# Kernel tuning notes

Measured on AMD Instinct MI355X. Metric: run time of the kernel, lower is better.

The kernel has to match this reference:

```python
import jax, jax.numpy as jnp
import numpy as np

N_NODES = 100000
N_EDGES = 1600000
D_IN = 128
D_OUT = 128


def setup_inputs() -> dict:
    key = jax.random.key(0)
    k = jax.random.split(key, 6)
    x = jax.random.normal(k[0], (N_NODES, D_IN), dtype=jnp.float32)
    edge_src = jax.random.randint(k[1], (N_EDGES,), 0, N_NODES, dtype=jnp.int64)
    edge_dst = jax.random.randint(k[2], (N_EDGES,), 0, N_NODES, dtype=jnp.int64)
    edge_weight = jax.random.uniform(k[3], (N_EDGES,), dtype=jnp.float32)
    # xavier-uniform-ish init for the two projection matrices
    lim = float(np.sqrt(6.0 / (D_IN + D_OUT)))
    W_nbrs = jax.random.uniform(k[4], (D_IN, D_OUT), minval=-lim, maxval=lim, dtype=jnp.float32)
    W_self = jax.random.uniform(k[5], (D_IN, D_OUT), minval=-lim, maxval=lim, dtype=jnp.float32)
    bias = jnp.zeros((D_OUT,), dtype=jnp.float32)
    return {"x": x, "edge_src": edge_src, "edge_dst": edge_dst,
            "edge_weight": edge_weight, "W_nbrs": W_nbrs, "W_self": W_self,
            "bias": bias}


def reference(x, edge_src, edge_dst, edge_weight, W_nbrs, W_self, bias):
    # y = x @ W_nbrs  (dense projection)
    y = x @ W_nbrs                                   # [N, D_OUT]
    # spmm(adj, y): out[i] = sum_{(j->i) in E} w_ij * y[j]
    msgs = edge_weight[:, None] * y[edge_src]        # [E, D_OUT]
    agg = jax.ops.segment_sum(msgs, edge_dst, num_segments=x.shape[0])
    # self transform + bias
    return agg + x @ W_self + bias
```

## Files before the change

### kernel.cpp

```cpp
#include <hip/hip_runtime.h>
#include <hip/hip_bf16.h>

#define D 128

typedef __bf16 bf16x8 __attribute__((ext_vector_type(8)));
typedef float f32x4 __attribute__((ext_vector_type(4)));

__device__ __forceinline__ unsigned short f2bf(float f) {
    unsigned u = __float_as_uint(f);
    u += 0x7FFFu + ((u >> 16) & 1u);
    return (unsigned short)(u >> 16);
}
__device__ __forceinline__ float bf2f(unsigned u16) {
    return __uint_as_float(u16 << 16);
}

__global__ void k_build_wt(const float* __restrict__ Wn, const float* __restrict__ Ws,
                           unsigned short* __restrict__ WTs) {
    int g = blockIdx.x * blockDim.x + threadIdx.x;
    int k = g >> 8;
    int c = g & 255;
    float v = (c < 128) ? Wn[k * 128 + c] : Ws[k * 128 + (c - 128)];
    int chunk = k >> 3;
    WTs[c * 128 + (((chunk ^ (c & 15)) << 3) | (k & 7))] = f2bf(v);
}

__global__ __launch_bounds__(256) void k_gemm_rank(
    const float* __restrict__ x, const unsigned short* __restrict__ WTs,
    const float* __restrict__ bias, int N,
    unsigned short* __restrict__ y, float* __restrict__ out,
    const int* __restrict__ edst, int E,
    int* __restrict__ cnt, int* __restrict__ rank) {
    __shared__ unsigned short sm[128 * 128];
    int b = blockIdx.x;
    int tid = threadIdx.x;
    if (b % 5 != 0) {
        int rb = (b / 5) * 4 + (b % 5) - 1;
        int e = rb * 256 + tid;
        if (e < E) {
            int d = edst[e];
            rank[e] = atomicAdd(&cnt[d], 1);
        }
        return;
    }
    int gb = b / 5;
    int w = tid >> 6, l = tid & 63;
    int row0 = gb * 64 + w * 16;
    if (gb * 64 >= N) return;
    int c15 = l & 15;
    int kgrp = l >> 4;
    const uint4* gs = (const uint4*)WTs;
    uint4* ss = (uint4*)sm;
    {
        #pragma unroll
        for (int r = 0; r < 8; ++r) ss[r * 256 + tid] = gs[r * 256 + tid];
    }
    int arow = row0 + c15;
    bool avalid = (arow < N);
    const float* xr = x + (size_t)arow * D;
    bf16x8 afrag[4];
    #pragma unroll
    for (int ks = 0; ks < 4; ++ks) {
        int k0 = ks * 32 + kgrp * 8;
        float4 a0, a1;
        if (avalid) { a0 = *(const float4*)(xr + k0); a1 = *(const float4*)(xr + k0 + 4); }
        else { a0 = make_float4(0.f, 0.f, 0.f, 0.f); a1 = a0; }
        bf16x8 f;
        f[0] = (__bf16)a0.x; f[1] = (__bf16)a0.y; f[2] = (__bf16)a0.z; f[3] = (__bf16)a0.w;
        f[4] = (__bf16)a1.x; f[5] = (__bf16)a1.y; f[6] = (__bf16)a1.z; f[7] = (__bf16)a1.w;
        afrag[ks] = f;
    }
    __syncthreads();
    int orow = row0 + kgrp * 4;
    #pragma unroll
    for (int nt = 0; nt < 8; ++nt) {
        int c = nt * 16 + c15;
        f32x4 acc = {0.f, 0.f, 0.f, 0.f};
        #pragma unroll
        for (int ks = 0; ks < 4; ++ks) {
            int chunk = ks * 4 + kgrp;
            const bf16x8* bp = (const bf16x8*)(sm + c * 128 + ((chunk ^ c15) << 3));
            acc = __builtin_amdgcn_mfma_f32_16x16x32_bf16(afrag[ks], *bp, acc, 0, 0, 0);
        }
        #pragma unroll
        for (int j = 0; j < 4; ++j) {
            int r = orow + j;
            if (r < N) y[(size_t)r * D + c] = f2bf(acc[j]);
        }
    }
    __syncthreads();
    {
        #pragma unroll
        for (int r = 0; r < 8; ++r) ss[r * 256 + tid] = gs[2048 + r * 256 + tid];
    }
    __syncthreads();
    #pragma unroll
    for (int nt = 0; nt < 8; ++nt) {
        int c = nt * 16 + c15;
        f32x4 acc = {0.f, 0.f, 0.f, 0.f};
        #pragma unroll
        for (int ks = 0; ks < 4; ++ks) {
            int chunk = ks * 4 + kgrp;
            const bf16x8* bp = (const bf16x8*)(sm + c * 128 + ((chunk ^ c15) << 3));
            acc = __builtin_amdgcn_mfma_f32_16x16x32_bf16(afrag[ks], *bp, acc, 0, 0, 0);
        }
        float bsv = bias[c];
        #pragma unroll
        for (int j = 0; j < 4; ++j) {
            int r = orow + j;
            if (r < N) out[(size_t)r * D + c] = acc[j] + bsv;
        }
    }
}

__global__ void k_scanA(const int* __restrict__ cnt, int N,
                        int* __restrict__ ofs, int* __restrict__ bsum) {
    __shared__ int lds[1024];
    int t = threadIdx.x, i = blockIdx.x * 1024 + t;
    int v = (i < N) ? cnt[i] : 0;
    lds[t] = v; __syncthreads();
    for (int d = 1; d < 1024; d <<= 1) {
        int x = (t >= d) ? lds[t - d] : 0; __syncthreads();
        lds[t] += x; __syncthreads();
    }
    if (i < N) ofs[i] = lds[t] - v;
    if (t == 1023) bsum[blockIdx.x] = lds[t];
}

__global__ void k_scanB(int* __restrict__ bsum, int NB) {
    __shared__ int lds[128];
    int t = threadIdx.x;
    int v = (t < NB) ? bsum[t] : 0;
    lds[t] = v; __syncthreads();
    for (int d = 1; d < 128; d <<= 1) {
        int x = (t >= d) ? lds[t - d] : 0; __syncthreads();
        lds[t] += x; __syncthreads();
    }
    if (t < NB) bsum[t] = lds[t] - v;
}

__global__ __launch_bounds__(256) void k_fill(
    const int* __restrict__ src, const int* __restrict__ dst,
    const float* __restrict__ w, const int* __restrict__ rank, int E,
    const int* __restrict__ ofs, const int* __restrict__ bsum,
    uint2* __restrict__ sorted) {
    int e = blockIdx.x * blockDim.x + threadIdx.x;
    if (e < E) {
        int d = dst[e];
        int pos = ofs[d] + bsum[d >> 10] + rank[e];
        sorted[pos] = make_uint2((unsigned)src[e], __float_as_uint(w[e]));
    }
}

__global__ __launch_bounds__(256) void k_agg(
    const unsigned short* __restrict__ y, const uint2* __restrict__ sorted,
    const int* __restrict__ ofs, const int* __restrict__ bsum,
    const int* __restrict__ cnt, int N,
    float* __restrict__ out) {
    int w = threadIdx.x >> 6, l = threadIdx.x & 63;
    int node = blockIdx.x * 4 + w;
    if (node >= N) return;
    int s = ofs[node] + bsum[node >> 10], n = cnt[node];
    int g = l >> 4, li = l & 15;
    const uint2* sp = sorted + s;
    float a0 = 0.f, a1 = 0.f, a2 = 0.f, a3 = 0.f;
    float a4 = 0.f, a5 = 0.f, a6 = 0.f, a7 = 0.f;
    int j = g;
    for (; j + 4 < n; j += 8) {
        uint2 pa = sp[j];
        uint2 pb = sp[j + 4];
        uint4 va = *(const uint4*)(y + (size_t)pa.x * D + li * 8);
        uint4 vb = *(const uint4*)(y + (size_t)pb.x * D + li * 8);
        float wa = __uint_as_float(pa.y), wb = __uint_as_float(pb.y);
        a0 += wa * bf2f(va.x & 0xFFFFu); a1 += wa * bf2f(va.x >> 16);
        a2 += wa * bf2f(va.y & 0xFFFFu); a3 += wa * bf2f(va.y >> 16);
        a4 += wa * bf2f(va.z & 0xFFFFu); a5 += wa * bf2f(va.z >> 16);
        a6 += wa * bf2f(va.w & 0xFFFFu); a7 += wa * bf2f(va.w >> 16);
        a0 += wb * bf2f(vb.x & 0xFFFFu); a1 += wb * bf2f(vb.x >> 16);
        a2 += wb * bf2f(vb.y & 0xFFFFu); a3 += wb * bf2f(vb.y >> 16);
        a4 += wb * bf2f(vb.z & 0xFFFFu); a5 += wb * bf2f(vb.z >> 16);
        a6 += wb * bf2f(vb.w & 0xFFFFu); a7 += wb * bf2f(vb.w >> 16);
    }
    if (j < n) {
        uint2 p = sp[j];
        uint4 v = *(const uint4*)(y + (size_t)p.x * D + li * 8);
        float wt = __uint_as_float(p.y);
        a0 += wt * bf2f(v.x & 0xFFFFu); a1 += wt * bf2f(v.x >> 16);
        a2 += wt * bf2f(v.y & 0xFFFFu); a3 += wt * bf2f(v.y >> 16);
        a4 += wt * bf2f(v.z & 0xFFFFu); a5 += wt * bf2f(v.z >> 16);
        a6 += wt * bf2f(v.w & 0xFFFFu); a7 += wt * bf2f(v.w >> 16);
    }
    a0 += __shfl_xor(a0, 16, 64); a1 += __shfl_xor(a1, 16, 64);
    a2 += __shfl_xor(a2, 16, 64); a3 += __shfl_xor(a3, 16, 64);
    a4 += __shfl_xor(a4, 16, 64); a5 += __shfl_xor(a5, 16, 64);
    a6 += __shfl_xor(a6, 16, 64); a7 += __shfl_xor(a7, 16, 64);
    a0 += __shfl_xor(a0, 32, 64); a1 += __shfl_xor(a1, 32, 64);
    a2 += __shfl_xor(a2, 32, 64); a3 += __shfl_xor(a3, 32, 64);
    a4 += __shfl_xor(a4, 32, 64); a5 += __shfl_xor(a5, 32, 64);
    a6 += __shfl_xor(a6, 32, 64); a7 += __shfl_xor(a7, 32, 64);
    if (l < 16) {
        float4* op = (float4*)(out + (size_t)node * D + li * 8);
        float4 o0 = op[0], o1 = op[1];
        o0.x += a0; o0.y += a1; o0.z += a2; o0.w += a3;
        o1.x += a4; o1.y += a5; o1.z += a6; o1.w += a7;
        op[0] = o0; op[1] = o1;
    }
}

extern "C" void kernel_launch(void* const* d_in, const int* in_sizes, int n_in,
                              void* d_out, int out_size, void* d_ws, size_t ws_size,
                              hipStream_t stream) {
    const float* x    = (const float*)d_in[0];
    const int*   esrc = (const int*)d_in[1];
    const int*   edst = (const int*)d_in[2];
    const float* ew   = (const float*)d_in[3];
    const float* Wn   = (const float*)d_in[4];
    const float* Wsf  = (const float*)d_in[5];
    const float* bias = (const float*)d_in[6];
    float* out = (float*)d_out;
    int N = in_sizes[0] / D;
    int E = in_sizes[1];

    char* ws = (char*)d_ws;
    size_t off = 0;
    unsigned short* WTs = (unsigned short*)(ws + off); off += 256 * 128 * sizeof(unsigned short);
    unsigned short* yb  = (unsigned short*)(ws + off); off += (size_t)N * D * sizeof(unsigned short);
    off = (off + 255) & ~(size_t)255;
    int* cnt  = (int*)(ws + off); off += (size_t)N * 4; off = (off + 255) & ~(size_t)255;
    int* ofs  = (int*)(ws + off); off += (size_t)N * 4; off = (off + 255) & ~(size_t)255;
    int* bsum = (int*)(ws + off); off += 1024;
    int* rank = (int*)(ws + off); off += (size_t)E * 4; off = (off + 255) & ~(size_t)255;
    uint2* sorted = (uint2*)(ws + off); off += (size_t)E * 8;

    hipMemsetAsync(cnt, 0, (size_t)N * 4, stream);

    k_build_wt<<<128, 256, 0, stream>>>(Wn, Wsf, WTs);

    int GB = (N + 63) / 64;
    int RB = (E + 255) / 256;
    int G5 = (GB > (RB + 3) / 4 ? GB : (RB + 3) / 4) * 5;
    k_gemm_rank<<<G5, 256, 0, stream>>>(x, WTs, bias, N, yb, out,
                                        edst, E, cnt, rank);

    int NB = (N + 1023) / 1024;
    k_scanA<<<NB, 1024, 0, stream>>>(cnt, N, ofs, bsum);
    k_scanB<<<1, 128, 0, stream>>>(bsum, NB);
    k_fill<<<(E + 255) / 256, 256, 0, stream>>>(esrc, edst, ew, rank, E, ofs, bsum, sorted);

    k_agg<<<(N + 3) / 4, 256, 0, stream>>>(yb, sorted, ofs, bsum, cnt, N, out);
}
```

Measured before the change: 304.0 us.

## Permute bf16 y columns for vector stores and stage output through LDS

The GEMM now stores the bf16 projection y in a permuted column order, so each lane writes 8 contiguous bf16 values as one vector store. The aggregation kernel's read-modify-write of out is changed to the matching strided column mapping. The self-transform output goes through LDS so it can be written with coalesced float4 stores that include the bias. The cnt memset is folded into the weight-transpose kernel, and the GEMM/rank block interleave changes from 1:4 to 1:1, with each rank block handling 1024 edges. The aim is fewer scattered narrow global stores and one fewer launch, at the cost of extra LDS traffic and syncs in the GEMM blocks.

```diff
diff --git a/kernel.cpp b/kernel.cpp
--- a/kernel.cpp
+++ b/kernel.cpp
@@ -4,6 +4,7 @@
 #define D 128
 
 typedef __bf16 bf16x8 __attribute__((ext_vector_type(8)));
+typedef unsigned short u16x8 __attribute__((ext_vector_type(8)));
 typedef float f32x4 __attribute__((ext_vector_type(4)));
 
 __device__ __forceinline__ unsigned short f2bf(float f) {
@@ -16,13 +17,15 @@
 }
 
 __global__ void k_build_wt(const float* __restrict__ Wn, const float* __restrict__ Ws,
-                           unsigned short* __restrict__ WTs) {
+                           unsigned short* __restrict__ WTs,
+                           int* __restrict__ cnt, int N) {
     int g = blockIdx.x * blockDim.x + threadIdx.x;
     int k = g >> 8;
     int c = g & 255;
     float v = (c < 128) ? Wn[k * 128 + c] : Ws[k * 128 + (c - 128)];
     int chunk = k >> 3;
     WTs[c * 128 + (((chunk ^ (c & 15)) << 3) | (k & 7))] = f2bf(v);
+    for (int i = g; i < N; i += 32768) cnt[i] = 0;
 }
 
 __global__ __launch_bounds__(256) void k_gemm_rank(
@@ -34,19 +37,23 @@
     __shared__ unsigned short sm[128 * 128];
     int b = blockIdx.x;
     int tid = threadIdx.x;
-    if (b % 5 != 0) {
-        int rb = (b / 5) * 4 + (b % 5) - 1;
-        int e = rb * 256 + tid;
-        if (e < E) {
-            int d = edst[e];
-            rank[e] = atomicAdd(&cnt[d], 1);
+    if (b & 1) {
+        int e0 = (b >> 1) * 1024 + tid;
+        #pragma unroll
+        for (int k = 0; k < 4; ++k) {
+            int e = e0 + k * 256;
+            if (e < E) {
+                int d = edst[e];
+                rank[e] = atomicAdd(&cnt[d], 1);
+            }
         }
         return;
     }
-    int gb = b / 5;
+    int gb = b >> 1;
+    int brow = gb * 64;
+    if (brow >= N) return;
     int w = tid >> 6, l = tid & 63;
-    int row0 = gb * 64 + w * 16;
-    if (gb * 64 >= N) return;
+    int row0 = brow + w * 16;
     int c15 = l & 15;
     int kgrp = l >> 4;
     const uint4* gs = (const uint4*)WTs;
@@ -72,20 +79,27 @@
     }
     __syncthreads();
     int orow = row0 + kgrp * 4;
+    f32x4 acc[8];
     #pragma unroll
     for (int nt = 0; nt < 8; ++nt) {
         int c = nt * 16 + c15;
-        f32x4 acc = {0.f, 0.f, 0.f, 0.f};
+        f32x4 a = {0.f, 0.f, 0.f, 0.f};
         #pragma unroll
         for (int ks = 0; ks < 4; ++ks) {
             int chunk = ks * 4 + kgrp;
             const bf16x8* bp = (const bf16x8*)(sm + c * 128 + ((chunk ^ c15) << 3));
-            acc = __builtin_amdgcn_mfma_f32_16x16x32_bf16(afrag[ks], *bp, acc, 0, 0, 0);
-        }
-        #pragma unroll
-        for (int j = 0; j < 4; ++j) {
-            int r = orow + j;
-            if (r < N) y[(size_t)r * D + c] = f2bf(acc[j]);
+            a = __builtin_amdgcn_mfma_f32_16x16x32_bf16(afrag[ks], *bp, a, 0, 0, 0);
+        }
+        acc[nt] = a;
+    }
+    #pragma unroll
+    for (int j = 0; j < 4; ++j) {
+        int r = orow + j;
+        if (r < N) {
+            u16x8 f;
+            #pragma unroll
+            for (int nt = 0; nt < 8; ++nt) f[nt] = f2bf(acc[nt][j]);
+            *(u16x8*)(y + (size_t)r * D + c15 * 8) = f;
         }
     }
     __syncthreads();
@@ -97,18 +111,34 @@
     #pragma unroll
     for (int nt = 0; nt < 8; ++nt) {
         int c = nt * 16 + c15;
-        f32x4 acc = {0.f, 0.f, 0.f, 0.f};
+        f32x4 a = {0.f, 0.f, 0.f, 0.f};
         #pragma unroll
         for (int ks = 0; ks < 4; ++ks) {
             int chunk = ks * 4 + kgrp;
             const bf16x8* bp = (const bf16x8*)(sm + c * 128 + ((chunk ^ c15) << 3));
-            acc = __builtin_amdgcn_mfma_f32_16x16x32_bf16(afrag[ks], *bp, acc, 0, 0, 0);
-        }
-        float bsv = bias[c];
-        #pragma unroll
-        for (int j = 0; j < 4; ++j) {
-            int r = orow + j;
-            if (r < N) out[(size_t)r * D + c] = acc[j] + bsv;
+            a = __builtin_amdgcn_mfma_f32_16x16x32_bf16(afrag[ks], *bp, a, 0, 0, 0);
+        }
+        acc[nt] = a;
+    }
+    __syncthreads();
+    float* smf = (float*)sm;
+    int lr0 = w * 16 + kgrp * 4;
+    #pragma unroll
+    for (int nt = 0; nt < 8; ++nt) {
+        #pragma unroll
+        for (int j = 0; j < 4; ++j)
+            smf[(lr0 + j) * 128 + nt * 16 + c15] = acc[nt][j];
+    }
+    __syncthreads();
+    float4 bv = *(const float4*)&bias[(tid * 4) & 127];
+    #pragma unroll
+    for (int k = 0; k < 8; ++k) {
+        int f = tid * 4 + k * 1024;
+        int gr = brow + (f >> 7);
+        if (gr < N) {
+            float4 c4 = *(float4*)&smf[f];
+            c4.x += bv.x; c4.y += bv.y; c4.z += bv.z; c4.w += bv.w;
+            *(float4*)(out + (size_t)brow * D + f) = c4;
         }
     }
 }
@@ -199,11 +229,9 @@
     a4 += __shfl_xor(a4, 32, 64); a5 += __shfl_xor(a5, 32, 64);
     a6 += __shfl_xor(a6, 32, 64); a7 += __shfl_xor(a7, 32, 64);
     if (l < 16) {
-        float4* op = (float4*)(out + (size_t)node * D + li * 8);
-        float4 o0 = op[0], o1 = op[1];
-        o0.x += a0; o0.y += a1; o0.z += a2; o0.w += a3;
-        o1.x += a4; o1.y += a5; o1.z += a6; o1.w += a7;
-        op[0] = o0; op[1] = o1;
+        float* op = out + (size_t)node * D + li;
+        op[0]   += a0; op[16]  += a1; op[32]  += a2; op[48]  += a3;
+        op[64]  += a4; op[80]  += a5; op[96]  += a6; op[112] += a7;
     }
 }
 
@@ -232,14 +260,12 @@
     int* rank = (int*)(ws + off); off += (size_t)E * 4; off = (off + 255) & ~(size_t)255;
     uint2* sorted = (uint2*)(ws + off); off += (size_t)E * 8;
 
-    hipMemsetAsync(cnt, 0, (size_t)N * 4, stream);
-
-    k_build_wt<<<128, 256, 0, stream>>>(Wn, Wsf, WTs);
+    k_build_wt<<<128, 256, 0, stream>>>(Wn, Wsf, WTs, cnt, N);
 
     int GB = (N + 63) / 64;
-    int RB = (E + 255) / 256;
-    int G5 = (GB > (RB + 3) / 4 ? GB : (RB + 3) / 4) * 5;
-    k_gemm_rank<<<G5, 256, 0, stream>>>(x, WTs, bias, N, yb, out,
+    int RB = (E + 1023) / 1024;
+    int G2 = (GB > RB ? GB : RB) * 2;
+    k_gemm_rank<<<G2, 256, 0, stream>>>(x, WTs, bias, N, yb, out,
                                         edst, E, cnt, rank);
 
     int NB = (N + 1023) / 1024;
```

New measurement: 293.3 us. -3.5%, faster.
